# Optimization experiments

Measured on AMD Instinct MI355X. Metric: run time of the kernel, lower is better.

Reference implementation:

```python
import jax, jax.numpy as jnp
import numpy as np

B, Q, L, D_LLM, D_KEYS = 2, 8, 2048, 768, 64
EPS = 1e-5

def setup_inputs() -> dict:
    key = jax.random.key(0)
    ks = jax.random.split(key, 7)
    s_in = 1.0 / np.sqrt(D_LLM)
    return {
        "info": jax.random.normal(ks[0], (B, Q, L, D_LLM), dtype=jnp.float32),
        "Wq": jax.random.uniform(ks[1], (D_LLM, D_KEYS), jnp.float32, -s_in, s_in),
        "bq": jax.random.uniform(ks[2], (D_KEYS,), jnp.float32, -s_in, s_in),
        "Wk": jax.random.uniform(ks[3], (D_LLM, D_KEYS), jnp.float32, -s_in, s_in),
        "bk": jax.random.uniform(ks[4], (D_KEYS,), jnp.float32, -s_in, s_in),
        "Wv": jax.random.uniform(ks[5], (D_LLM, D_KEYS), jnp.float32, -s_in, s_in),
        "bv": jax.random.uniform(ks[6], (D_KEYS,), jnp.float32, -s_in, s_in),
    }

def reference(info, Wq, bq, Wk, bk, Wv, bv):
    # Projections: [B,Q,L,d_llm] @ [d_llm,d_keys] -> [B,Q,L,E]
    q = info @ Wq + bq
    k = info @ Wk + bk
    v = info @ Wv + bv
    E = q.shape[-1]
    scale = 1.0 / jnp.sqrt(jnp.asarray(E, dtype=q.dtype))
    # Full L x L score tensor per (b,q) slice, as in the original einsum path
    scores = jnp.einsum('bqle,bqme->bqlm', q, k)
    A = jax.nn.softmax(scale * scores, axis=-1)  # dropout is identity at eval
    out = jnp.einsum('bqlm,bqme->bqle', A, v)    # [B,Q,L,E]
    # InstanceNorm2d (no affine): normalize each (b,q) slice over (L,E)
    mu = jnp.mean(out, axis=(2, 3), keepdims=True)
    var = jnp.var(out, axis=(2, 3), keepdims=True)  # biased variance
    return (out - mu) / jnp.sqrt(var + EPS)
```

## Files before the change

kernel.cpp:

```cpp
#include <hip/hip_runtime.h>
#include <math.h>

#define L_SEQ   2048
#define DLLM    768
#define E_DIM   64
#define NSLICE  16
#define EPSV    1e-5f
#define LSTR    72

typedef _Float16 f16;
typedef _Float16 f16x8 __attribute__((ext_vector_type(8)));
typedef _Float16 f16x4 __attribute__((ext_vector_type(4)));
typedef float    f32x4 __attribute__((ext_vector_type(4)));

__global__ __launch_bounds__(256)
void prep_kernel(const float* __restrict__ Wq, const float* __restrict__ bq,
                 const float* __restrict__ Wk, const float* __restrict__ bk,
                 const float* __restrict__ Wv, const float* __restrict__ bv,
                 f16* __restrict__ Wt, float* __restrict__ bias)
{
    int b = blockIdx.x;
    if (b < 192) {
        int sel = b >> 6, c = b & 63;
        const float* W = (sel == 0) ? Wq : (sel == 1) ? Wk : Wv;
        float s = (sel == 0) ? 0.125f : 1.0f;
        for (int kd = threadIdx.x; kd < DLLM; kd += 256)
            Wt[b * DLLM + kd] = (f16)(W[kd * 64 + c] * s);
    } else {
        int t = threadIdx.x;
        if (t < 192) {
            int sel = t >> 6, c = t & 63;
            const float* bb = (sel == 0) ? bq : (sel == 1) ? bk : bv;
            bias[t] = bb[c] * ((sel == 0) ? 0.125f : 1.0f);
        }
    }
}

__global__ __launch_bounds__(256)
void proj_mfma(const float* __restrict__ info, const f16* __restrict__ Wt,
               const float* __restrict__ bias,
               f16* __restrict__ q16, f16* __restrict__ k16, f16* __restrict__ vT)
{
    __shared__ f16 As[2][64 * LSTR];
    __shared__ f16 Bs[2][192 * LSTR];

    const int tid = threadIdx.x;
    const int l   = tid & 63;
    const int wid = tid >> 6;
    const int l15 = l & 15, lg = l >> 4;
    const int wm  = (wid >> 1) * 32;
    const int wn  = (wid & 1) * 96;
    const int r0  = blockIdx.x * 64;
    const int srow = tid >> 3;
    const int sc8  = tid & 7;

    f32x4 acc[2][6];
    #pragma unroll
    for (int mi = 0; mi < 2; ++mi)
        #pragma unroll
        for (int ni = 0; ni < 6; ++ni) acc[mi][ni] = (f32x4)(0.0f);

    float4 fa[2][2];
    f16x8  gb[6];

    #pragma unroll
    for (int u = 0; u < 2; ++u) {
        const float* src = info + (size_t)(r0 + u * 32 + srow) * DLLM + sc8 * 8;
        fa[u][0] = *reinterpret_cast<const float4*>(src);
        fa[u][1] = *reinterpret_cast<const float4*>(src + 4);
    }
    #pragma unroll
    for (int u = 0; u < 6; ++u)
        gb[u] = *reinterpret_cast<const f16x8*>(
            Wt + (size_t)(u * 32 + srow) * DLLM + sc8 * 8);

    #pragma unroll
    for (int u = 0; u < 2; ++u) {
        f16x8 h;
        #pragma unroll
        for (int j = 0; j < 4; ++j) {
            h[j]     = (f16)(&fa[u][0].x)[j];
            h[j + 4] = (f16)(&fa[u][1].x)[j];
        }
        *reinterpret_cast<f16x8*>(&As[0][(u * 32 + srow) * LSTR + sc8 * 8]) = h;
    }
    #pragma unroll
    for (int u = 0; u < 6; ++u)
        *reinterpret_cast<f16x8*>(&Bs[0][(u * 32 + srow) * LSTR + sc8 * 8]) = gb[u];
    __syncthreads();

    for (int ks = 0; ks < 12; ++ks) {
        const int cur = ks & 1;
        const int kn  = (ks + 1) * 64;
        if (ks < 11) {
            #pragma unroll
            for (int u = 0; u < 2; ++u) {
                const float* src = info + (size_t)(r0 + u * 32 + srow) * DLLM + kn + sc8 * 8;
                fa[u][0] = *reinterpret_cast<const float4*>(src);
                fa[u][1] = *reinterpret_cast<const float4*>(src + 4);
            }
            #pragma unroll
            for (int u = 0; u < 6; ++u)
                gb[u] = *reinterpret_cast<const f16x8*>(
                    Wt + (size_t)(u * 32 + srow) * DLLM + kn + sc8 * 8);
        }

        const f16* Ac = As[cur];
        const f16* Bc = Bs[cur];
        #pragma unroll
        for (int kf = 0; kf < 2; ++kf) {
            f16x8 af[2], bf[6];
            #pragma unroll
            for (int mi = 0; mi < 2; ++mi)
                af[mi] = *reinterpret_cast<const f16x8*>(
                    &Ac[(wm + mi * 16 + l15) * LSTR + kf * 32 + lg * 8]);
            #pragma unroll
            for (int ni = 0; ni < 6; ++ni)
                bf[ni] = *reinterpret_cast<const f16x8*>(
                    &Bc[(wn + ni * 16 + l15) * LSTR + kf * 32 + lg * 8]);
            #pragma unroll
            for (int mi = 0; mi < 2; ++mi)
                #pragma unroll
                for (int ni = 0; ni < 6; ++ni)
                    acc[mi][ni] = __builtin_amdgcn_mfma_f32_16x16x32_f16(
                        af[mi], bf[ni], acc[mi][ni], 0, 0, 0);
        }

        if (ks < 11) {
            f16* An = As[cur ^ 1];
            f16* Bn = Bs[cur ^ 1];
            #pragma unroll
            for (int u = 0; u < 2; ++u) {
                f16x8 h;
                #pragma unroll
                for (int j = 0; j < 4; ++j) {
                    h[j]     = (f16)(&fa[u][0].x)[j];
                    h[j + 4] = (f16)(&fa[u][1].x)[j];
                }
                *reinterpret_cast<f16x8*>(&An[(u * 32 + srow) * LSTR + sc8 * 8]) = h;
            }
            #pragma unroll
            for (int u = 0; u < 6; ++u)
                *reinterpret_cast<f16x8*>(&Bn[(u * 32 + srow) * LSTR + sc8 * 8]) = gb[u];
        }
        __syncthreads();
    }

    #pragma unroll
    for (int ni = 0; ni < 6; ++ni) {
        const int nb  = wn + ni * 16;
        const int n   = nb + l15;
        const int sel = nb >> 6;
        const int cc  = (nb & 63) + l15;
        const float bcol = bias[n];
        if (sel < 2) {
            f16* dst = (sel == 0) ? q16 : k16;
            #pragma unroll
            for (int mi = 0; mi < 2; ++mi)
                #pragma unroll
                for (int rr = 0; rr < 4; ++rr) {
                    int r = r0 + wm + mi * 16 + lg * 4 + rr;
                    dst[(size_t)r * E_DIM + cc] = (f16)(acc[mi][ni][rr] + bcol);
                }
        } else {
            #pragma unroll
            for (int mi = 0; mi < 2; ++mi) {
                int rb    = r0 + wm + mi * 16 + lg * 4;
                int slice = rb >> 11;
                int lloc  = rb & 2047;
                f16x4 v4;
                #pragma unroll
                for (int rr = 0; rr < 4; ++rr) v4[rr] = (f16)(acc[mi][ni][rr] + bcol);
                *reinterpret_cast<f16x4*>(
                    vT + (size_t)slice * E_DIM * L_SEQ + (size_t)cc * L_SEQ + lloc) = v4;
            }
        }
    }
}

__global__ __launch_bounds__(256)
void attn_mfma(const f16* __restrict__ q16, const f16* __restrict__ k16,
               const f16* __restrict__ vT, float* __restrict__ att)
{
    __shared__ f16 Ks[2][64 * LSTR];
    __shared__ f16 Vs[2][64 * LSTR];
    __shared__ f16 Pl[4 * 16 * LSTR];

    const int tid = threadIdx.x;
    const int l   = tid & 63;
    const int wid = tid >> 6;
    const int l15 = l & 15, lg = l >> 4;
    const int slice = blockIdx.y;
    const int q0 = blockIdx.x * 64 + wid * 16;
    const f16* qp = q16 + (size_t)slice * L_SEQ * E_DIM;
    const f16* kp = k16 + (size_t)slice * L_SEQ * E_DIM;
    const f16* vp = vT  + (size_t)slice * E_DIM * L_SEQ;
    f16* P = &Pl[wid * 16 * LSTR];
    const int srow = tid >> 3;
    const int sc8  = tid & 7;

    f16x8 qf[2];
    #pragma unroll
    for (int kf = 0; kf < 2; ++kf)
        qf[kf] = *reinterpret_cast<const f16x8*>(
            qp + (size_t)(q0 + l15) * E_DIM + kf * 32 + lg * 8);

    f32x4 oacc[4];
    #pragma unroll
    for (int ei = 0; ei < 4; ++ei) oacc[ei] = (f32x4)(0.0f);
    float M = -1e30f, Lr = 0.f;

    f16x8 gk[2], gv[2];
    #pragma unroll
    for (int u = 0; u < 2; ++u) {
        int row = u * 32 + srow;
        gk[u] = *reinterpret_cast<const f16x8*>(kp + (size_t)row * E_DIM + sc8 * 8);
        gv[u] = *reinterpret_cast<const f16x8*>(vp + (size_t)row * L_SEQ + sc8 * 8);
    }
    #pragma unroll
    for (int u = 0; u < 2; ++u) {
        int row = u * 32 + srow;
        *reinterpret_cast<f16x8*>(&Ks[0][row * LSTR + sc8 * 8]) = gk[u];
        *reinterpret_cast<f16x8*>(&Vs[0][row * LSTR + sc8 * 8]) = gv[u];
    }
    __syncthreads();

    for (int ch = 0; ch < 32; ++ch) {
        const int cur = ch & 1;
        const int kvn = (ch + 1) * 64;
        if (ch < 31) {
            #pragma unroll
            for (int u = 0; u < 2; ++u) {
                int row = u * 32 + srow;
                gk[u] = *reinterpret_cast<const f16x8*>(
                    kp + (size_t)(kvn + row) * E_DIM + sc8 * 8);
                gv[u] = *reinterpret_cast<const f16x8*>(
                    vp + (size_t)row * L_SEQ + kvn + sc8 * 8);
            }
        }

        const f16* Kc = Ks[cur];
        const f16* Vc = Vs[cur];

        f32x4 s[4];
        #pragma unroll
        for (int ni = 0; ni < 4; ++ni) s[ni] = (f32x4)(0.0f);
        #pragma unroll
        for (int kf = 0; kf < 2; ++kf)
            #pragma unroll
            for (int ni = 0; ni < 4; ++ni) {
                f16x8 kb = *reinterpret_cast<const f16x8*>(
                    &Kc[(ni * 16 + l15) * LSTR + kf * 32 + lg * 8]);
                s[ni] = __builtin_amdgcn_mfma_f32_16x16x32_f16(kb, qf[kf], s[ni], 0, 0, 0);
            }

        float mx = -1e30f;
        #pragma unroll
        for (int ni = 0; ni < 4; ++ni)
            #pragma unroll
            for (int r = 0; r < 4; ++r) mx = fmaxf(mx, s[ni][r]);
        mx = fmaxf(mx, __shfl_xor(mx, 16));
        mx = fmaxf(mx, __shfl_xor(mx, 32));
        float Mn  = fmaxf(M, mx);
        float fsc = __expf(M - Mn);
        M = Mn;
        float psum = 0.f;
        #pragma unroll
        for (int ni = 0; ni < 4; ++ni) {
            f16x4 p4;
            #pragma unroll
            for (int r = 0; r < 4; ++r) {
                float p = __expf(s[ni][r] - Mn);
                psum += p;
                p4[r] = (f16)p;
            }
            *reinterpret_cast<f16x4*>(&P[l15 * LSTR + ni * 16 + lg * 4]) = p4;
        }
        Lr = Lr * fsc + psum;
        #pragma unroll
        for (int ei = 0; ei < 4; ++ei) {
            oacc[ei][0] *= fsc; oacc[ei][1] *= fsc;
            oacc[ei][2] *= fsc; oacc[ei][3] *= fsc;
        }

        #pragma unroll
        for (int kf = 0; kf < 2; ++kf) {
            f16x8 pa = *reinterpret_cast<const f16x8*>(
                &P[l15 * LSTR + kf * 32 + lg * 8]);
            #pragma unroll
            for (int ei = 0; ei < 4; ++ei) {
                f16x8 vb = *reinterpret_cast<const f16x8*>(
                    &Vc[(ei * 16 + l15) * LSTR + kf * 32 + lg * 8]);
                oacc[ei] = __builtin_amdgcn_mfma_f32_16x16x32_f16(vb, pa, oacc[ei], 0, 0, 0);
            }
        }

        if (ch < 31) {
            f16* Kn = Ks[cur ^ 1];
            f16* Vn = Vs[cur ^ 1];
            #pragma unroll
            for (int u = 0; u < 2; ++u) {
                int row = u * 32 + srow;
                *reinterpret_cast<f16x8*>(&Kn[row * LSTR + sc8 * 8]) = gk[u];
                *reinterpret_cast<f16x8*>(&Vn[row * LSTR + sc8 * 8]) = gv[u];
            }
        }
        __syncthreads();
    }

    float lt = Lr;
    lt += __shfl_xor(lt, 16);
    lt += __shfl_xor(lt, 32);
    float inv = 1.f / lt;
    size_t row = (size_t)slice * L_SEQ + q0 + l15;
    #pragma unroll
    for (int ei = 0; ei < 4; ++ei) {
        float4 o;
        o.x = oacc[ei][0] * inv; o.y = oacc[ei][1] * inv;
        o.z = oacc[ei][2] * inv; o.w = oacc[ei][3] * inv;
        *reinterpret_cast<float4*>(att + row * E_DIM + ei * 16 + lg * 4) = o;
    }
}

__global__ __launch_bounds__(256)
void stats_kernel(const float* __restrict__ att, float* __restrict__ parts)
{
    const int slice = blockIdx.x >> 4;
    const int part  = blockIdx.x & 15;
    const int tid = threadIdx.x;
    const size_t base = (size_t)slice * L_SEQ * E_DIM + (size_t)part * 8192;
    float s = 0.f, sq = 0.f;
    #pragma unroll
    for (int it = 0; it < 8; ++it) {
        float4 v = *reinterpret_cast<const float4*>(att + base + (size_t)(it * 256 + tid) * 4);
        s  += v.x + v.y + v.z + v.w;
        sq += v.x * v.x + v.y * v.y + v.z * v.z + v.w * v.w;
    }
    for (int m = 1; m < 64; m <<= 1) {
        s  += __shfl_xor(s,  m);
        sq += __shfl_xor(sq, m);
    }
    __shared__ float red[8];
    const int wid = tid >> 6;
    if ((tid & 63) == 0) { red[wid * 2] = s; red[wid * 2 + 1] = sq; }
    __syncthreads();
    if (tid == 0) {
        parts[slice * 32 + part * 2]     = red[0] + red[2] + red[4] + red[6];
        parts[slice * 32 + part * 2 + 1] = red[1] + red[3] + red[5] + red[7];
    }
}

__global__ __launch_bounds__(256)
void apply_kernel(float* __restrict__ att, const float* __restrict__ parts)
{
    const int i4 = blockIdx.x * 256 + threadIdx.x;
    const size_t fl = (size_t)i4 * 4;
    const int slice = (int)(fl >> 17);
    float S = 0.f, SQ = 0.f;
    #pragma unroll
    for (int p = 0; p < 16; ++p) {
        S  += parts[slice * 32 + p * 2];
        SQ += parts[slice * 32 + p * 2 + 1];
    }
    const float N = (float)(L_SEQ * E_DIM);
    float mean = S / N;
    float var  = SQ / N - mean * mean;
    float inv  = rsqrtf(var + EPSV);
    float4 v = *reinterpret_cast<const float4*>(att + fl);
    float4 o;
    o.x = (v.x - mean) * inv;
    o.y = (v.y - mean) * inv;
    o.z = (v.z - mean) * inv;
    o.w = (v.w - mean) * inv;
    *reinterpret_cast<float4*>(att + fl) = o;
}

extern "C" void kernel_launch(void* const* d_in, const int* in_sizes, int n_in,
                              void* d_out, int out_size, void* d_ws, size_t ws_size,
                              hipStream_t stream)
{
    const float* info = (const float*)d_in[0];
    const float* Wq   = (const float*)d_in[1];
    const float* bq   = (const float*)d_in[2];
    const float* Wk   = (const float*)d_in[3];
    const float* bk   = (const float*)d_in[4];
    const float* Wv   = (const float*)d_in[5];
    const float* bv   = (const float*)d_in[6];

    char* ws = (char*)d_ws;
    f16*   Wt    = (f16*)(ws);
    float* bias  = (float*)(ws + 294912);
    float* parts = (float*)(ws + 295936);
    f16*   q16   = (f16*)(ws + 1048576);
    f16*   k16   = (f16*)(ws + 5242880);
    f16*   vT    = (f16*)(ws + 9437184);
    float* att   = (float*)d_out;

    prep_kernel<<<193, 256, 0, stream>>>(Wq, bq, Wk, bk, Wv, bv, Wt, bias);
    proj_mfma<<<512, 256, 0, stream>>>(info, Wt, bias, q16, k16, vT);
    attn_mfma<<<dim3(L_SEQ / 64, NSLICE), 256, 0, stream>>>(q16, k16, vT, att);
    stats_kernel<<<256, 256, 0, stream>>>(att, parts);
    apply_kernel<<<2048, 256, 0, stream>>>(att, parts);
}
```

Baseline: 222.3 us.

## Enlarge attention blocks, add lazy softmax rescale and MFMA priority, tile weight prep

The attention kernel now uses 512-thread blocks covering 128 queries each, so one K/V chunk load in shared memory is shared by twice as many query rows, and each thread stages a single row. The online softmax skips rescaling the output accumulators unless the running max grows by more than 8, saving the exp and multiplies on most chunks at some cost in numeric headroom. s_setprio is raised around the MFMA sections. The weight prep kernel switches to a coalesced shared-memory transpose with 36 blocks instead of strided scalar reads.

```diff
diff --git a/kernel.cpp b/kernel.cpp
--- a/kernel.cpp
+++ b/kernel.cpp
@@ -19,20 +19,40 @@
                  const float* __restrict__ Wv, const float* __restrict__ bv,
                  f16* __restrict__ Wt, float* __restrict__ bias)
 {
-    int b = blockIdx.x;
-    if (b < 192) {
-        int sel = b >> 6, c = b & 63;
-        const float* W = (sel == 0) ? Wq : (sel == 1) ? Wk : Wv;
-        float s = (sel == 0) ? 0.125f : 1.0f;
-        for (int kd = threadIdx.x; kd < DLLM; kd += 256)
-            Wt[b * DLLM + kd] = (f16)(W[kd * 64 + c] * s);
-    } else {
-        int t = threadIdx.x;
-        if (t < 192) {
-            int sel = t >> 6, c = t & 63;
-            const float* bb = (sel == 0) ? bq : (sel == 1) ? bk : bv;
-            bias[t] = bb[c] * ((sel == 0) ? 0.125f : 1.0f);
-        }
+    __shared__ float tile[64][69];
+    const int tid = threadIdx.x;
+    const int mat = blockIdx.x / 12;
+    const int k0  = (blockIdx.x % 12) * 64;
+    const float* W = (mat == 0) ? Wq : (mat == 1) ? Wk : Wv;
+    const float scale = (mat == 0) ? 0.125f : 1.0f;
+
+    #pragma unroll
+    for (int u = 0; u < 4; ++u) {
+        int r  = u * 16 + (tid >> 4);
+        int c4 = tid & 15;
+        float4 v = *reinterpret_cast<const float4*>(W + (size_t)(k0 + r) * 64 + c4 * 4);
+        tile[r][c4 * 4 + 0] = v.x;
+        tile[r][c4 * 4 + 1] = v.y;
+        tile[r][c4 * 4 + 2] = v.z;
+        tile[r][c4 * 4 + 3] = v.w;
+    }
+    __syncthreads();
+
+    #pragma unroll
+    for (int p = 0; p < 2; ++p) {
+        int c   = p * 32 + (tid >> 3);
+        int sc8 = tid & 7;
+        f16x8 h;
+        #pragma unroll
+        for (int j = 0; j < 8; ++j)
+            h[j] = (f16)(tile[sc8 * 8 + j][c] * scale);
+        *reinterpret_cast<f16x8*>(
+            Wt + (size_t)(mat * 64 + c) * DLLM + k0 + sc8 * 8) = h;
+    }
+
+    if ((blockIdx.x % 12) == 0 && tid < 64) {
+        const float* bb = (mat == 0) ? bq : (mat == 1) ? bk : bv;
+        bias[mat * 64 + tid] = bb[tid] * scale;
     }
 }
 
@@ -178,20 +198,20 @@
     }
 }
 
-__global__ __launch_bounds__(256)
+__global__ __launch_bounds__(512, 4)
 void attn_mfma(const f16* __restrict__ q16, const f16* __restrict__ k16,
                const f16* __restrict__ vT, float* __restrict__ att)
 {
     __shared__ f16 Ks[2][64 * LSTR];
     __shared__ f16 Vs[2][64 * LSTR];
-    __shared__ f16 Pl[4 * 16 * LSTR];
+    __shared__ f16 Pl[8 * 16 * LSTR];
 
     const int tid = threadIdx.x;
     const int l   = tid & 63;
     const int wid = tid >> 6;
     const int l15 = l & 15, lg = l >> 4;
     const int slice = blockIdx.y;
-    const int q0 = blockIdx.x * 64 + wid * 16;
+    const int q0 = blockIdx.x * 128 + wid * 16;
     const f16* qp = q16 + (size_t)slice * L_SEQ * E_DIM;
     const f16* kp = k16 + (size_t)slice * L_SEQ * E_DIM;
     const f16* vp = vT  + (size_t)slice * E_DIM * L_SEQ;
@@ -210,33 +230,21 @@
     for (int ei = 0; ei < 4; ++ei) oacc[ei] = (f32x4)(0.0f);
     float M = -1e30f, Lr = 0.f;
 
-    f16x8 gk[2], gv[2];
-    #pragma unroll
-    for (int u = 0; u < 2; ++u) {
-        int row = u * 32 + srow;
-        gk[u] = *reinterpret_cast<const f16x8*>(kp + (size_t)row * E_DIM + sc8 * 8);
-        gv[u] = *reinterpret_cast<const f16x8*>(vp + (size_t)row * L_SEQ + sc8 * 8);
-    }
-    #pragma unroll
-    for (int u = 0; u < 2; ++u) {
-        int row = u * 32 + srow;
-        *reinterpret_cast<f16x8*>(&Ks[0][row * LSTR + sc8 * 8]) = gk[u];
-        *reinterpret_cast<f16x8*>(&Vs[0][row * LSTR + sc8 * 8]) = gv[u];
-    }
+    f16x8 gk, gv;
+    gk = *reinterpret_cast<const f16x8*>(kp + (size_t)srow * E_DIM + sc8 * 8);
+    gv = *reinterpret_cast<const f16x8*>(vp + (size_t)srow * L_SEQ + sc8 * 8);
+    *reinterpret_cast<f16x8*>(&Ks[0][srow * LSTR + sc8 * 8]) = gk;
+    *reinterpret_cast<f16x8*>(&Vs[0][srow * LSTR + sc8 * 8]) = gv;
     __syncthreads();
 
     for (int ch = 0; ch < 32; ++ch) {
         const int cur = ch & 1;
         const int kvn = (ch + 1) * 64;
         if (ch < 31) {
-            #pragma unroll
-            for (int u = 0; u < 2; ++u) {
-                int row = u * 32 + srow;
-                gk[u] = *reinterpret_cast<const f16x8*>(
-                    kp + (size_t)(kvn + row) * E_DIM + sc8 * 8);
-                gv[u] = *reinterpret_cast<const f16x8*>(
-                    vp + (size_t)row * L_SEQ + kvn + sc8 * 8);
-            }
+            gk = *reinterpret_cast<const f16x8*>(
+                kp + (size_t)(kvn + srow) * E_DIM + sc8 * 8);
+            gv = *reinterpret_cast<const f16x8*>(
+                vp + (size_t)srow * L_SEQ + kvn + sc8 * 8);
         }
 
         const f16* Kc = Ks[cur];
@@ -245,6 +253,7 @@
         f32x4 s[4];
         #pragma unroll
         for (int ni = 0; ni < 4; ++ni) s[ni] = (f32x4)(0.0f);
+        __builtin_amdgcn_s_setprio(1);
         #pragma unroll
         for (int kf = 0; kf < 2; ++kf)
             #pragma unroll
@@ -253,6 +262,7 @@
                     &Kc[(ni * 16 + l15) * LSTR + kf * 32 + lg * 8]);
                 s[ni] = __builtin_amdgcn_mfma_f32_16x16x32_f16(kb, qf[kf], s[ni], 0, 0, 0);
             }
+        __builtin_amdgcn_s_setprio(0);
 
         float mx = -1e30f;
         #pragma unroll
@@ -261,28 +271,32 @@
             for (int r = 0; r < 4; ++r) mx = fmaxf(mx, s[ni][r]);
         mx = fmaxf(mx, __shfl_xor(mx, 16));
         mx = fmaxf(mx, __shfl_xor(mx, 32));
-        float Mn  = fmaxf(M, mx);
-        float fsc = __expf(M - Mn);
-        M = Mn;
+        if (!__all(mx <= M + 8.f)) {
+            float Mn  = fmaxf(M, mx);
+            float fsc = __expf(M - Mn);
+            M = Mn;
+            Lr *= fsc;
+            #pragma unroll
+            for (int ei = 0; ei < 4; ++ei) {
+                oacc[ei][0] *= fsc; oacc[ei][1] *= fsc;
+                oacc[ei][2] *= fsc; oacc[ei][3] *= fsc;
+            }
+        }
         float psum = 0.f;
         #pragma unroll
         for (int ni = 0; ni < 4; ++ni) {
             f16x4 p4;
             #pragma unroll
             for (int r = 0; r < 4; ++r) {
-                float p = __expf(s[ni][r] - Mn);
+                float p = __expf(s[ni][r] - M);
                 psum += p;
                 p4[r] = (f16)p;
             }
             *reinterpret_cast<f16x4*>(&P[l15 * LSTR + ni * 16 + lg * 4]) = p4;
         }
-        Lr = Lr * fsc + psum;
-        #pragma unroll
-        for (int ei = 0; ei < 4; ++ei) {
-            oacc[ei][0] *= fsc; oacc[ei][1] *= fsc;
-            oacc[ei][2] *= fsc; oacc[ei][3] *= fsc;
-        }
-
+        Lr += psum;
+
+        __builtin_amdgcn_s_setprio(1);
         #pragma unroll
         for (int kf = 0; kf < 2; ++kf) {
             f16x8 pa = *reinterpret_cast<const f16x8*>(
@@ -294,16 +308,13 @@
                 oacc[ei] = __builtin_amdgcn_mfma_f32_16x16x32_f16(vb, pa, oacc[ei], 0, 0, 0);
             }
         }
+        __builtin_amdgcn_s_setprio(0);
 
         if (ch < 31) {
             f16* Kn = Ks[cur ^ 1];
             f16* Vn = Vs[cur ^ 1];
-            #pragma unroll
-            for (int u = 0; u < 2; ++u) {
-                int row = u * 32 + srow;
-                *reinterpret_cast<f16x8*>(&Kn[row * LSTR + sc8 * 8]) = gk[u];
-                *reinterpret_cast<f16x8*>(&Vn[row * LSTR + sc8 * 8]) = gv[u];
-            }
+            *reinterpret_cast<f16x8*>(&Kn[srow * LSTR + sc8 * 8]) = gk;
+            *reinterpret_cast<f16x8*>(&Vn[srow * LSTR + sc8 * 8]) = gv;
         }
         __syncthreads();
     }
@@ -396,9 +407,9 @@
     f16*   vT    = (f16*)(ws + 9437184);
     float* att   = (float*)d_out;
 
-    prep_kernel<<<193, 256, 0, stream>>>(Wq, bq, Wk, bk, Wv, bv, Wt, bias);
+    prep_kernel<<<36, 256, 0, stream>>>(Wq, bq, Wk, bk, Wv, bv, Wt, bias);
     proj_mfma<<<512, 256, 0, stream>>>(info, Wt, bias, q16, k16, vT);
-    attn_mfma<<<dim3(L_SEQ / 64, NSLICE), 256, 0, stream>>>(q16, k16, vT, att);
+    attn_mfma<<<dim3(L_SEQ / 128, NSLICE), 512, 0, stream>>>(q16, k16, vT, att);
     stats_kernel<<<256, 256, 0, stream>>>(att, parts);
     apply_kernel<<<2048, 256, 0, stream>>>(att, parts);
 }
```

After: 217.6 us. -2.1%, faster.
